# Kernel optimization log

Measured on AMD Instinct MI355X. Metric: run time of the kernel, lower is better.

## Reference

```python
import jax, jax.numpy as jnp
import numpy as np

B, A, C, H, W = 16, 5, 512, 16, 16


def _affine_grid(theta, Hh, Ww):
    # torch F.affine_grid, align_corners=False (default). theta: [2,3]
    xs = (2.0 * jnp.arange(Ww, dtype=jnp.float32) + 1.0) / Ww - 1.0  # [W]
    ys = (2.0 * jnp.arange(Hh, dtype=jnp.float32) + 1.0) / Hh - 1.0  # [H]
    gx = theta[0, 0] * xs[None, :] + theta[0, 1] * ys[:, None] + theta[0, 2]  # [H,W]
    gy = theta[1, 0] * xs[None, :] + theta[1, 1] * ys[:, None] + theta[1, 2]  # [H,W]
    return gx, gy


def _grid_sample(img, gx, gy):
    # torch F.grid_sample, bilinear, padding_mode='zeros', align_corners=False
    # img: [C,H,W]; gx,gy: [H,W] normalized coords
    C_, Hh, Ww = img.shape
    ix = ((gx + 1.0) * Ww - 1.0) * 0.5
    iy = ((gy + 1.0) * Hh - 1.0) * 0.5
    x0 = jnp.floor(ix); y0 = jnp.floor(iy)
    x1 = x0 + 1.0;      y1 = y0 + 1.0
    wx1 = ix - x0; wx0 = 1.0 - wx1
    wy1 = iy - y0; wy0 = 1.0 - wy1

    def gather(xi, yi):
        inb = (xi >= 0) & (xi < Ww) & (yi >= 0) & (yi < Hh)
        xc = jnp.clip(xi, 0, Ww - 1).astype(jnp.int32)
        yc = jnp.clip(yi, 0, Hh - 1).astype(jnp.int32)
        return img[:, yc, xc] * inb[None].astype(img.dtype)  # [C,H,W]

    return (gather(x0, y0) * (wx0 * wy0)[None] + gather(x1, y0) * (wx1 * wy0)[None]
          + gather(x0, y1) * (wx0 * wy1)[None] + gather(x1, y1) * (wx1 * wy1)[None])


def _warp(nb_feat, nb_warp):
    # nb_feat: [C,H,W] neighbor feature; nb_warp: [4,4] pose matrix
    zero = jnp.zeros((), dtype=jnp.float32)
    one = jnp.ones((), dtype=jnp.float32)
    theta_rot = jnp.stack([
        jnp.stack([nb_warp[0, 0], nb_warp[0, 1], zero]),
        jnp.stack([nb_warp[1, 0], nb_warp[1, 1], zero])])  # [2,3]
    gx_r, gy_r = _affine_grid(theta_rot, H, W)
    feat_rot = _grid_sample(nb_feat, gx_r, gy_r)
    x_trans = 4.0 * nb_warp[0, 3] / 128.0
    y_trans = -(4.0 * nb_warp[1, 3]) / 128.0
    theta_trans = jnp.stack([
        jnp.stack([one, zero, x_trans]),
        jnp.stack([zero, one, y_trans])])
    gx_t, gy_t = _affine_grid(theta_trans, H, W)
    return _grid_sample(feat_rot, gx_t, gy_t)  # [C,H,W]


def _fuse_one(local_b, trans_b, n):
    # local_b: [A,C,H,W], trans_b: [A,A,4,4], n: scalar num_agent
    # pair[i,j] = warp of agent j's feature into agent i's frame
    pair = jax.vmap(lambda t_i: jax.vmap(_warp)(local_b, t_i))(trans_b)  # [A,A,C,H,W]
    idx = jnp.arange(A)
    mask = (idx[:, None] != idx[None, :]) & (idx[:, None] < n) & (idx[None, :] < n)
    return local_b + jnp.einsum('ij,ijchw->ichw', mask.astype(local_b.dtype), pair)


def setup_inputs() -> dict:
    key = jax.random.key(0)
    k1, k2, k3, k4 = jax.random.split(key, 4)
    feat_maps = jax.random.normal(k1, (A * B, C, H, W), dtype=jnp.float32)
    # realistic near-rigid pose matrices: rotation block + translation column
    ang = jax.random.uniform(k2, (B, A, A), minval=-0.5, maxval=0.5)
    tr = jax.random.normal(k3, (B, A, A, 2), dtype=jnp.float32) * 8.0
    tm = jnp.zeros((B, A, A, 4, 4), dtype=jnp.float32)
    tm = tm.at[..., 0, 0].set(jnp.cos(ang)).at[..., 0, 1].set(-jnp.sin(ang))
    tm = tm.at[..., 1, 0].set(jnp.sin(ang)).at[..., 1, 1].set(jnp.cos(ang))
    tm = tm.at[..., 0, 3].set(tr[..., 0]).at[..., 1, 3].set(tr[..., 1])
    tm = tm.at[..., 2, 2].set(1.0).at[..., 3, 3].set(1.0)
    num_agent = jax.random.randint(k4, (B, A), 1, 6, dtype=jnp.int64) if jax.config.jax_enable_x64 else jax.random.randint(k4, (B, A), 1, 6, dtype=jnp.int32)
    return {"feat_maps": feat_maps, "trans_matrices": tm, "num_agent_tensor": num_agent}


def reference(feat_maps, trans_matrices, num_agent_tensor):
    # feat_maps is agent-major blocks of size B (feat_maps[B*i:B*(i+1)] is agent i)
    local = feat_maps.reshape(A, B, C, H, W).transpose(1, 0, 2, 3, 4)  # [B,A,C,H,W]
    fused = jax.vmap(_fuse_one)(local, trans_matrices, num_agent_tensor[:, 0])
    # agents2batch: concat agents along batch dim -> [A*B,C,H,W]
    return fused.transpose(1, 0, 2, 3, 4).reshape(A * B, C, H, W)
```

## Files before the change

kernel.cpp:

```cpp
#include <hip/hip_runtime.h>

#define NB 16
#define NA 5
#define NC 512
#define HW 256
#define NCG 8
#define NITEMS (NA * NB * NCG)

typedef float f4 __attribute__((ext_vector_type(4)));
typedef _Float16 h8 __attribute__((ext_vector_type(8)));

static __device__ __forceinline__ h8 splat8(float v) {
    const _Float16 h = (_Float16)v;
    h8 r = {h, h, h, h, h, h, h, h};
    return r;
}

__global__ __launch_bounds__(256) void fafmimo_amort_kernel(
    const float* __restrict__ feat,
    const float* __restrict__ trans,
    const int*   __restrict__ numa,
    float*       __restrict__ out)
{
    __shared__ h8 slab[8][HW];

    const int idx = blockIdx.x;
    const int i   = idx % NA;
    const int b   = (idx / NA) % NB;
    const int cg  = idx / (NA * NB);
    const int c0  = cg * 64;
    const int px  = threadIdx.x;
    const int x   = px & 15, y = px >> 4;
    const int n   = numa[b * NA];
    const bool work = (i < n) && (n > 1);

    h8 acc[8];
#pragma unroll
    for (int ch = 0; ch < 8; ++ch) acc[ch] = splat8(0.0f);

    if (work) {
        bool dirty = false;
        for (int jj = 0; jj < 4; ++jj) {
            const int j = jj + (jj >= i);
            if (j < n) {
                const float* src = feat + ((size_t)(j * NB + b) * NC + c0) * HW + px;
                if (dirty) __syncthreads();
#pragma unroll
                for (int half = 0; half < 2; ++half) {
                    float tmp[32];
#pragma unroll
                    for (int k = 0; k < 32; ++k) tmp[k] = src[(half * 32 + k) * HW];
#pragma unroll
                    for (int cq = 0; cq < 4; ++cq) {
                        h8 v;
#pragma unroll
                        for (int k = 0; k < 8; ++k) v[k] = (_Float16)tmp[cq * 8 + k];
                        slab[half * 4 + cq][px] = v;
                    }
                }
                __syncthreads();
                dirty = true;

                const float* tb = trans + (size_t)(((b * NA) + i) * NA + j) * 16;
                const f4 row0 = *(const f4*)tb;
                const f4 row1 = *(const f4*)(tb + 4);
                const float r00 = row0.x, r01 = row0.y;
                const float r10 = row1.x, r11 = row1.y;

                int   ta[16];
                float wa[16];
                {
                    const float dx = 0.25f * row0.w;
                    const float dy = -0.25f * row1.w;
                    const float fdx = floorf(dx), fdy = floorf(dy);
                    const float tx1 = dx - fdx, tx0 = 1.0f - tx1;
                    const float ty1 = dy - fdy, ty0 = 1.0f - ty1;
                    const int ox = x + (int)fdx;
                    const int oy = y + (int)fdy;
                    const float fox = (float)ox - 7.5f;
                    const float foy = (float)oy - 7.5f;
                    const float bxr = r00 * fox + r01 * foy + 7.5f;
                    const float byr = r10 * fox + r11 * foy + 7.5f;
                    int t = 0;
#pragma unroll
                    for (int sy = 0; sy < 2; ++sy)
#pragma unroll
                    for (int sx = 0; sx < 2; ++sx) {
                        const int tox = ox + sx, toy = oy + sy;
                        const bool in2 = (tox >= 0) && (tox < 16) && (toy >= 0) && (toy < 16);
                        const float ws = in2 ? (sx ? tx1 : tx0) * (sy ? ty1 : ty0) : 0.0f;
                        const float cx = bxr + (float)sx * r00 + (float)sy * r01;
                        const float cy = byr + (float)sx * r10 + (float)sy * r11;
                        const float fx0 = floorf(cx), fy0 = floorf(cy);
                        const float wx1 = cx - fx0, wy1 = cy - fy0;
                        const int ix0 = (int)fx0, iy0 = (int)fy0;
                        const float mx0 = (ix0 >= 0 && ix0 < 16) ? 1.0f - wx1 : 0.0f;
                        const float mx1 = (ix0 + 1 >= 0 && ix0 + 1 < 16) ? wx1 : 0.0f;
                        const float my0 = ((iy0 >= 0 && iy0 < 16) ? 1.0f - wy1 : 0.0f) * ws;
                        const float my1 = ((iy0 + 1 >= 0 && iy0 + 1 < 16) ? wy1 : 0.0f) * ws;
                        const int cx0 = min(max(ix0, 0), 15), cx1 = min(max(ix0 + 1, 0), 15);
                        const int cy0 = min(max(iy0, 0), 15), cy1 = min(max(iy0 + 1, 0), 15);
                        ta[t] = cy0 * 16 + cx0; wa[t++] = mx0 * my0;
                        ta[t] = cy0 * 16 + cx1; wa[t++] = mx1 * my0;
                        ta[t] = cy1 * 16 + cx0; wa[t++] = mx0 * my1;
                        ta[t] = cy1 * 16 + cx1; wa[t++] = mx1 * my1;
                    }
                }

#pragma unroll
                for (int t = 0; t < 16; ++t) {
                    const h8 W = splat8(wa[t]);
                    const h8* sp = &slab[0][ta[t]];
#pragma unroll
                    for (int ch = 0; ch < 8; ++ch)
                        acc[ch] += sp[ch * HW] * W;
                }
            }
        }
    }

    const size_t obase = ((size_t)(i * NB + b) * NC + c0) * HW + px;
    const float* own = feat + obase;
    float* dst = out + obase;
#pragma unroll
    for (int ch = 0; ch < 8; ++ch)
#pragma unroll
        for (int k = 0; k < 8; ++k)
            dst[(ch * 8 + k) * HW] = own[(ch * 8 + k) * HW] + (float)acc[ch][k];
}

extern "C" void kernel_launch(void* const* d_in, const int* in_sizes, int n_in,
                              void* d_out, int out_size, void* d_ws, size_t ws_size,
                              hipStream_t stream) {
    const float* feat  = (const float*)d_in[0];
    const float* trans = (const float*)d_in[1];
    const int*   numa  = (const int*)d_in[2];
    float* out = (float*)d_out;

    fafmimo_amort_kernel<<<dim3(NITEMS), dim3(256), 0, stream>>>(
        feat, trans, numa, out);
}
```

Before: 112.0 us.

## Restructure blocks to share all agents' 8-channel slabs across every receiver agent

```diff
diff --git a/kernel.cpp b/kernel.cpp
--- a/kernel.cpp
+++ b/kernel.cpp
@@ -4,8 +4,8 @@
 #define NA 5
 #define NC 512
 #define HW 256
-#define NCG 8
-#define NITEMS (NA * NB * NCG)
+#define NCHG 64
+#define NBLK (NB * NCHG)
 
 typedef float f4 __attribute__((ext_vector_type(4)));
 typedef _Float16 h8 __attribute__((ext_vector_type(8)));
@@ -16,50 +16,55 @@
     return r;
 }
 
-__global__ __launch_bounds__(256) void fafmimo_amort_kernel(
+__global__ __launch_bounds__(256) void fafmimo_strip_kernel(
     const float* __restrict__ feat,
     const float* __restrict__ trans,
     const int*   __restrict__ numa,
     float*       __restrict__ out)
 {
-    __shared__ h8 slab[8][HW];
+    __shared__ h8 slab[NA][HW];
 
-    const int idx = blockIdx.x;
-    const int i   = idx % NA;
-    const int b   = (idx / NA) % NB;
-    const int cg  = idx / (NA * NB);
-    const int c0  = cg * 64;
-    const int px  = threadIdx.x;
-    const int x   = px & 15, y = px >> 4;
+    const int blk = blockIdx.x;
+    const int b   = blk & (NB - 1);
+    const int g   = blk >> 4;
+    const int c0  = g << 3;
+    const int tid = threadIdx.x;
+    const int w   = tid >> 6;
+    const int l   = tid & 63;
     const int n   = numa[b * NA];
-    const bool work = (i < n) && (n > 1);
 
-    h8 acc[8];
+    if (n > 1) {
+        for (int j = w; j < n; j += 4) {
+            const float* src = feat + ((size_t)(j * NB + b) * NC + c0) * HW + 4 * l;
+            f4 t[8];
 #pragma unroll
-    for (int ch = 0; ch < 8; ++ch) acc[ch] = splat8(0.0f);
+            for (int k = 0; k < 8; ++k) t[k] = *(const f4*)(src + k * HW);
+#pragma unroll
+            for (int m = 0; m < 4; ++m) {
+                h8 hv;
+#pragma unroll
+                for (int k = 0; k < 8; ++k) hv[k] = (_Float16)t[k][m];
+                slab[j][4 * l + m] = hv;
+            }
+        }
+    }
+    __syncthreads();
 
-    if (work) {
-        bool dirty = false;
-        for (int jj = 0; jj < 4; ++jj) {
-            const int j = jj + (jj >= i);
-            if (j < n) {
-                const float* src = feat + ((size_t)(j * NB + b) * NC + c0) * HW + px;
-                if (dirty) __syncthreads();
+    for (int s = w; s < 20; s += 4) {
+        const int i  = s >> 2;
+        const int q  = s & 3;
+        const int px = (q << 6) + l;
+        const int x  = px & 15, y = px >> 4;
+        const size_t base = ((size_t)(i * NB + b) * NC + c0) * HW + px;
+
+        float own[8];
 #pragma unroll
-                for (int half = 0; half < 2; ++half) {
-                    float tmp[32];
-#pragma unroll
-                    for (int k = 0; k < 32; ++k) tmp[k] = src[(half * 32 + k) * HW];
-#pragma unroll
-                    for (int cq = 0; cq < 4; ++cq) {
-                        h8 v;
-#pragma unroll
-                        for (int k = 0; k < 8; ++k) v[k] = (_Float16)tmp[cq * 8 + k];
-                        slab[half * 4 + cq][px] = v;
-                    }
-                }
-                __syncthreads();
-                dirty = true;
+        for (int k = 0; k < 8; ++k) own[k] = feat[base + k * HW];
+
+        h8 pacc = splat8(0.0f);
+        if (i < n && n > 1) {
+            for (int j = 0; j < n; ++j) {
+                if (j == i) continue;
 
                 const float* tb = trans + (size_t)(((b * NA) + i) * NA + j) * 16;
                 const f4 row0 = *(const f4*)tb;
@@ -107,26 +112,19 @@
                     }
                 }
 
+                const h8* sj = &slab[j][0];
+                h8 tv[16];
 #pragma unroll
-                for (int t = 0; t < 16; ++t) {
-                    const h8 W = splat8(wa[t]);
-                    const h8* sp = &slab[0][ta[t]];
+                for (int t = 0; t < 16; ++t) tv[t] = sj[ta[t]];
 #pragma unroll
-                    for (int ch = 0; ch < 8; ++ch)
-                        acc[ch] += sp[ch * HW] * W;
-                }
+                for (int t = 0; t < 16; ++t) pacc += tv[t] * splat8(wa[t]);
             }
         }
+
+        float* dst = out + base;
+#pragma unroll
+        for (int k = 0; k < 8; ++k) dst[k * HW] = own[k] + (float)pacc[k];
     }
-
-    const size_t obase = ((size_t)(i * NB + b) * NC + c0) * HW + px;
-    const float* own = feat + obase;
-    float* dst = out + obase;
-#pragma unroll
-    for (int ch = 0; ch < 8; ++ch)
-#pragma unroll
-        for (int k = 0; k < 8; ++k)
-            dst[(ch * 8 + k) * HW] = own[(ch * 8 + k) * HW] + (float)acc[ch][k];
 }
 
 extern "C" void kernel_launch(void* const* d_in, const int* in_sizes, int n_in,
@@ -137,6 +135,6 @@
     const int*   numa  = (const int*)d_in[2];
     float* out = (float*)d_out;
 
-    fafmimo_amort_kernel<<<dim3(NITEMS), dim3(256), 0, stream>>>(
+    fafmimo_strip_kernel<<<dim3(NBLK), dim3(256), 0, stream>>>(
         feat, trans, numa, out);
 }
```

New measurement: 131.6 us. 17.5% more time.
